# Kernel optimization log

Measured on AMD Instinct MI355X. Metric: run time of the kernel, lower is better.

Reference implementation:

```python
import jax, jax.numpy as jnp
import numpy as np
from jax import lax

B, H, W = 4096, 15, 15
P, V = 16, 32
D = P + V            # 48
PCODE = 2380
NEMB = 2 * (PCODE + 1)  # 4762


def _conv(x, w, b=None, groups=1, pad='SAME'):
    # x: [B,C,H,W], w: [O, I/groups, kh, kw] (torch OIHW layout)
    y = lax.conv_general_dilated(
        x, w, window_strides=(1, 1), padding=pad,
        dimension_numbers=('NCHW', 'OIHW', 'NCHW'),
        feature_group_count=groups)
    if b is not None:
        y = y + b[None, :, None, None]
    return y


def setup_inputs() -> dict:
    key = jax.random.key(0)
    ks = jax.random.split(key, 18)
    f = lambda k, shape: (jax.random.normal(k, shape, jnp.float32) * 0.05)
    inp = {
        'emb': f(ks[0], (NEMB, D)),
        'conv_w': f(ks[1], (D, 1, 3, 3)),      # depthwise, groups=D
        'conv_b': f(ks[2], (D,)),
        'ppw_w': f(ks[3], (P, P, 1, 1)),
        'ppw_b': f(ks[4], (P,)),
        'pdw_w': f(ks[5], (P, 1, 3, 3)),       # depthwise, groups=P
        'pdw_b': f(ks[6], (P,)),
        'pf_w': f(ks[7], (1, P, 1, 1)),        # final policy conv, no bias
        'vpw_w': f(ks[8], (V, V, 1, 1)),
        'vpw_b': f(ks[9], (V,)),
        'vl1_w': f(ks[10], (V, V)),
        'vl1_b': f(ks[11], (V,)),
        'vl2_w': f(ks[12], (V, V)),
        'vl2_b': f(ks[13], (V,)),
        'vf_w': f(ks[14], (3, V)),
        'vf_b': f(ks[15], (3,)),
        'sparse_feature_input': jax.random.randint(ks[16], (B, 12, H, W), 0, PCODE, jnp.int32),
        'board_input': jax.random.randint(ks[17], (B, 2, H, W), 0, 2, jnp.int32),
    }
    return inp


def reference(emb, conv_w, conv_b, ppw_w, ppw_b, pdw_w, pdw_b, pf_w,
              vpw_w, vpw_b, vl1_w, vl1_b, vl2_w, vl2_b, vf_w, vf_b,
              sparse_feature_input, board_input):
    relu = jax.nn.relu
    # --- PatternCodeEmbedding ---
    pcode = sparse_feature_input[:, 10:12]                     # [B,2,H,W]
    pcode = jnp.where(board_input > 0, PCODE, pcode)
    pcode = pcode + jnp.array([0, PCODE + 1], jnp.int32)[None, :, None, None]
    feat = emb[pcode].sum(axis=1)                              # [B,H,W,D]
    feat = jnp.transpose(feat, (0, 3, 1, 2))                   # [B,D,H,W]
    # --- trunk depthwise conv ---
    feat = relu(_conv(feat, conv_w, conv_b, groups=D))
    # --- policy head ---
    pol = feat[:, :P]
    pol = relu(_conv(pol, ppw_w, ppw_b))
    pol = relu(_conv(pol, pdw_w, pdw_b, groups=P))
    pol = _conv(pol, pf_w)                                     # [B,1,H,W]
    # --- value head ---
    val = feat[:, P:]
    val = relu(_conv(val, vpw_w, vpw_b))
    val = jnp.mean(val, axis=(2, 3))                           # [B,V]
    val = relu(val @ vl1_w.T + vl1_b)
    val = relu(val @ vl2_w.T + vl2_b)
    val = val @ vf_w.T + vf_b                                  # [B,3]
    return val, pol
```

## Files before the change

### kernel.cpp

```cpp
#include <hip/hip_runtime.h>
#include <hip/hip_fp16.h>

typedef _Float16 half8  __attribute__((ext_vector_type(8)));
typedef _Float16 half4_t __attribute__((ext_vector_type(4)));
typedef _Float16 half2_t __attribute__((ext_vector_type(2)));
typedef float f32x4 __attribute__((ext_vector_type(4)));

namespace {
constexpr int NT = 256;
constexpr int NPIX = 225;
constexpr int PCODE_C = 2380;

constexpr int AROW = 272;
constexpr int ACG  = 4080;

constexpr int OFF_A     = 0;
constexpr int OFF_POLA0 = 0;
constexpr int OFF_XLO   = 12240;
constexpr int OFF_SV    = 23040;
constexpr int OFF_H1    = 23168;
constexpr int OFF_H2    = 23296;
constexpr int OFF_XHI   = 24480;
constexpr int OFF_ZROW  = 35280;
constexpr int OFF_WS    = 35392;
constexpr int OFF_SLOTP = 36352;
constexpr int SMEM_BYTES = 36672;
}

__device__ __forceinline__ half2_t pkrtz(float a, float b) {
    return __builtin_bit_cast(half2_t, __builtin_amdgcn_cvt_pkrtz(a, b));
}
__device__ __forceinline__ void wave_fence() {
    asm volatile("s_waitcnt lgkmcnt(0)" ::: "memory");
}

__global__ __launch_bounds__(NT, 4) void patnet_kernel(
    const float* __restrict__ emb,
    const float* __restrict__ conv_w, const float* __restrict__ conv_b,
    const float* __restrict__ ppw_w,  const float* __restrict__ ppw_b,
    const float* __restrict__ pdw_w,  const float* __restrict__ pdw_b,
    const float* __restrict__ pf_w,
    const float* __restrict__ vpw_w,  const float* __restrict__ vpw_b,
    const float* __restrict__ vl1_w,  const float* __restrict__ vl1_b,
    const float* __restrict__ vl2_w,  const float* __restrict__ vl2_b,
    const float* __restrict__ vf_w,   const float* __restrict__ vf_b,
    const int* __restrict__ sparse,   const int* __restrict__ board,
    float* __restrict__ out, int batch)
{
    __shared__ __align__(16) unsigned char smem[SMEM_BYTES];
    const int tid  = threadIdx.x;
    const int b    = blockIdx.x;
    const int lane = tid & 63;
    const int wave = tid >> 6;

    int c0 = 0, c1 = 0;
    if (tid < NPIX) {
        int s10 = sparse[b * 2700 + 10 * NPIX + tid];
        int s11 = sparse[b * 2700 + 11 * NPIX + tid];
        int b0  = board[b * 450 + tid];
        int b1  = board[b * 450 + NPIX + tid];
        c0 = (b0 > 0) ? PCODE_C : s10;
        c1 = ((b1 > 0) ? PCODE_C : s11) + (PCODE_C + 1);
    }

    {
        _Float16* WS = (_Float16*)(smem + OFF_WS);
        for (int i = tid; i < 480; i += NT) {
            int cg = i / 80, r = i - cg * 80;
            _Float16 v;
            if (r < 72) { int t = r >> 3, j = r & 7; v = (_Float16)conv_w[(cg * 8 + j) * 9 + t]; }
            else        { v = (_Float16)conv_b[cg * 8 + (r - 72)]; }
            WS[i] = v;
        }
        _Float16* WP = (_Float16*)(smem + OFF_SLOTP);
        if (tid < 160) {
            int cg = tid / 80, r = tid - cg * 80;
            _Float16 v;
            if (r < 72) { int t = r >> 3, j = r & 7; v = (_Float16)pdw_w[(cg * 8 + j) * 9 + t]; }
            else        { v = (_Float16)pdw_b[cg * 8 + (r - 72)]; }
            WP[tid] = v;
        }
        if (tid < 187) {
            unsigned char* dst;
            if (tid < 180) {
                int cg = tid / 30, r = tid - cg * 30;
                int row = r >> 1, colB = (r & 1) * 256;
                dst = smem + OFF_A + cg * ACG + row * AROW + colB;
            } else {
                dst = smem + OFF_ZROW + (tid - 180) * 16;
            }
            *(half8*)dst = (half8)(_Float16)0.f;
        }
    }

    if (tid < NPIX) {
        const float* e0 = emb + c0 * 48;
        const float* e1 = emb + c1 * 48;
        int y = tid / 15, x = tid - y * 15;
        unsigned char* abase = smem + OFF_A + y * AROW + (x + 1) * 16;
        #pragma unroll
        for (int g = 0; g < 6; g++) {
            f32x4 x0 = *(const f32x4*)(e0 + g * 8);
            f32x4 x1 = *(const f32x4*)(e0 + g * 8 + 4);
            f32x4 y0 = *(const f32x4*)(e1 + g * 8);
            f32x4 y1 = *(const f32x4*)(e1 + g * 8 + 4);
            f32x4 s0 = x0 + y0, s1 = x1 + y1;
            half2_t q0 = pkrtz(s0.x, s0.y), q1 = pkrtz(s0.z, s0.w);
            half2_t q2 = pkrtz(s1.x, s1.y), q3 = pkrtz(s1.z, s1.w);
            half8 hv = {q0[0], q0[1], q1[0], q1[1], q2[0], q2[1], q3[0], q3[1]};
            *(half8*)(abase + g * ACG) = hv;
        }
    }
    __syncthreads();

    auto do_strip = [&](int t, int cgbase, int xBase) {
        int cgl = t / 75, rem = t - cgl * 75;
        int y = rem / 5, s = rem - y * 5;
        int cg = cgbase + cgl;
        const unsigned char* wb = smem + OFF_WS + cg * 160;
        half8 wv[9];
        #pragma unroll
        for (int i = 0; i < 9; i++) wv[i] = *(const half8*)(wb + i * 16);
        half8 bias = *(const half8*)(wb + 144);
        const unsigned char* abase = smem + OFF_A + cg * ACG;
        int xo = s * 48;
        const unsigned char* r0 = (y >= 1)  ? abase + (y - 1) * AROW + xo : smem + OFF_ZROW;
        const unsigned char* r1 = abase + y * AROW + xo;
        const unsigned char* r2 = (y <= 13) ? abase + (y + 1) * AROW + xo : smem + OFF_ZROW;
        half8 acc[3] = {bias, bias, bias};
        #pragma unroll
        for (int c = 0; c < 5; c++) {
            half8 v0 = *(const half8*)(r0 + c * 16);
            half8 v1 = *(const half8*)(r1 + c * 16);
            half8 v2 = *(const half8*)(r2 + c * 16);
            #pragma unroll
            for (int o = 0; o < 3; o++) {
                int kx = c - o;
                if (kx >= 0 && kx <= 2) {
                    acc[o] = __builtin_elementwise_fma(v0, wv[kx],     acc[o]);
                    acc[o] = __builtin_elementwise_fma(v1, wv[3 + kx], acc[o]);
                    acc[o] = __builtin_elementwise_fma(v2, wv[6 + kx], acc[o]);
                }
            }
        }
        unsigned char* xw = smem + xBase + (y * 15 + s * 3) * 48 + cgl * 16;
        #pragma unroll
        for (int o = 0; o < 3; o++)
            *(half8*)(xw + o * 48) = __builtin_elementwise_max(acc[o], (half8)(_Float16)0.f);
    };

    if (tid < 225) do_strip(tid, 3, OFF_XHI);
    __syncthreads();
    if (tid < 225) do_strip(tid, 0, OFF_XLO);

    const int n = lane & 15, q = lane >> 4;
    const int cgp = lane & 1;
    half8 af_p;
    {
        const float* wp = ppw_w + n * 16 + (q & 1) * 8;
        f32x4 w0 = *(const f32x4*)wp, w1 = *(const f32x4*)(wp + 4);
        half8 t = {(_Float16)w0.x, (_Float16)w0.y, (_Float16)w0.z, (_Float16)w0.w,
                   (_Float16)w1.x, (_Float16)w1.y, (_Float16)w1.z, (_Float16)w1.w};
        af_p = (q < 2) ? t : (half8)(_Float16)0.f;
    }
    f32x4 pb = *(const f32x4*)(ppw_b + q * 4);
    half2_t pf0 = pkrtz(pf_w[cgp * 8 + 0], pf_w[cgp * 8 + 1]);
    half2_t pf1 = pkrtz(pf_w[cgp * 8 + 2], pf_w[cgp * 8 + 3]);
    half2_t pf2 = pkrtz(pf_w[cgp * 8 + 4], pf_w[cgp * 8 + 5]);
    half2_t pf3 = pkrtz(pf_w[cgp * 8 + 6], pf_w[cgp * 8 + 7]);
    half8 af0, af1;
    {
        const float* wp = vpw_w + n * 32 + q * 8;
        f32x4 w0 = *(const f32x4*)wp, w1 = *(const f32x4*)(wp + 4);
        af0 = half8{(_Float16)w0.x, (_Float16)w0.y, (_Float16)w0.z, (_Float16)w0.w,
                    (_Float16)w1.x, (_Float16)w1.y, (_Float16)w1.z, (_Float16)w1.w};
        const float* wp2 = vpw_w + (16 + n) * 32 + q * 8;
        f32x4 v0 = *(const f32x4*)wp2, v1 = *(const f32x4*)(wp2 + 4);
        af1 = half8{(_Float16)v0.x, (_Float16)v0.y, (_Float16)v0.z, (_Float16)v0.w,
                    (_Float16)v1.x, (_Float16)v1.y, (_Float16)v1.z, (_Float16)v1.w};
    }
    f32x4 vb0 = *(const f32x4*)(vpw_b + q * 4);
    f32x4 vb1 = *(const f32x4*)(vpw_b + 16 + q * 4);
    __syncthreads();

    if (wave < 3) {
        if (lane < 60) {
            int cg = lane / 30, r = lane - cg * 30;
            int row = r >> 1, colB = (r & 1) * 256;
            *(half8*)(smem + OFF_POLA0 + cg * ACG + row * AROW + colB) = (half8)(_Float16)0.f;
        }
        half8 wvp[9];
        #pragma unroll
        for (int t = 0; t < 9; t++) wvp[t] = *(const half8*)(smem + OFF_SLOTP + cgp * 160 + t * 16);
        half8 biasp = *(const half8*)(smem + OFF_SLOTP + cgp * 160 + 144);

        const int tlo = (wave == 0) ? 0 : ((wave == 1) ? 3 : 8);
        const int thi = (wave == 0) ? 6 : ((wave == 1) ? 11 : 15);
        const int cg3 = q >> 1;
        const int xoff = (q & 1) * 16;
        for (int t = tlo; t < thi; t++) {
            int p = t * 16 + n;
            int pc = (p > 224) ? 224 : p;
            half8 bf = *(const half8*)(smem + OFF_XLO + pc * 48 + xoff);
            f32x4 d = __builtin_amdgcn_mfma_f32_16x16x32_f16(af_p, bf, (f32x4)(0.f), 0, 0, 0);
            if (p < NPIX) {
                int y = p / 15, x = p - y * 15;
                half2_t lo = pkrtz(fmaxf(d.x + pb.x, 0.f), fmaxf(d.y + pb.y, 0.f));
                half2_t hi = pkrtz(fmaxf(d.z + pb.z, 0.f), fmaxf(d.w + pb.w, 0.f));
                half4_t hv = {lo[0], lo[1], hi[0], hi[1]};
                *(half4_t*)(smem + OFF_POLA0 + cg3 * ACG + y * AROW + (x + 1) * 16 + (q & 1) * 8) = hv;
            }
        }
        wave_fence();

        const int px0 = wave * 75;
        for (int i = 0; i < 3; i++) {
            int idx = i * 64 + lane;
            if (idx < 150) {
                int px = px0 + (idx >> 1);
                int y = px / 15, x = px - y * 15;
                const unsigned char* base = smem + OFF_POLA0 + cgp * ACG;
                int xo = x * 16;
                const unsigned char* pm = (y > 0)  ? base + (y - 1) * AROW + xo : smem + OFF_ZROW;
                const unsigned char* pz = base + y * AROW + xo;
                const unsigned char* pp = (y < 14) ? base + (y + 1) * AROW + xo : smem + OFF_ZROW;
                half8 acc = biasp;
                acc = __builtin_elementwise_fma(*(const half8*)(pm),      wvp[0], acc);
                acc = __builtin_elementwise_fma(*(const half8*)(pm + 16), wvp[1], acc);
                acc = __builtin_elementwise_fma(*(const half8*)(pm + 32), wvp[2], acc);
                acc = __builtin_elementwise_fma(*(const half8*)(pz),      wvp[3], acc);
                acc = __builtin_elementwise_fma(*(const half8*)(pz + 16), wvp[4], acc);
                acc = __builtin_elementwise_fma(*(const half8*)(pz + 32), wvp[5], acc);
                acc = __builtin_elementwise_fma(*(const half8*)(pp),      wvp[6], acc);
                acc = __builtin_elementwise_fma(*(const half8*)(pp + 16), wvp[7], acc);
                acc = __builtin_elementwise_fma(*(const half8*)(pp + 32), wvp[8], acc);
                acc = __builtin_elementwise_max(acc, (half8)(_Float16)0.f);
                float part = 0.f;
                part = __builtin_amdgcn_fdot2(half2_t{acc[0], acc[1]}, pf0, part, false);
                part = __builtin_amdgcn_fdot2(half2_t{acc[2], acc[3]}, pf1, part, false);
                part = __builtin_amdgcn_fdot2(half2_t{acc[4], acc[5]}, pf2, part, false);
                part = __builtin_amdgcn_fdot2(half2_t{acc[6], acc[7]}, pf3, part, false);
                float tot = part + __shfl_xor(part, 1, 64);
                if (cgp == 0) out[3 * batch + b * NPIX + px] = tot;
            }
        }
    } else {
        const int xb = (q == 0) ? (OFF_XLO + 32) : (OFF_XHI + (q - 1) * 16);
        f32x4 a0 = {0.f, 0.f, 0.f, 0.f}, a1 = {0.f, 0.f, 0.f, 0.f};
        for (int t = 0; t < 15; t++) {
            int p = t * 16 + n;
            int pc = (p > 224) ? 224 : p;
            half8 bf = *(const half8*)(smem + xb + pc * 48);
            f32x4 d0 = __builtin_amdgcn_mfma_f32_16x16x32_f16(af0, bf, (f32x4)(0.f), 0, 0, 0);
            f32x4 d1 = __builtin_amdgcn_mfma_f32_16x16x32_f16(af1, bf, (f32x4)(0.f), 0, 0, 0);
            if (p < NPIX) {
                #pragma unroll
                for (int r = 0; r < 4; r++) {
                    a0[r] += fmaxf(d0[r] + vb0[r], 0.f);
                    a1[r] += fmaxf(d1[r] + vb1[r], 0.f);
                }
            }
        }
        #pragma unroll
        for (int s = 1; s < 16; s <<= 1) {
            #pragma unroll
            for (int r = 0; r < 4; r++) {
                a0[r] += __shfl_xor(a0[r], s, 64);
                a1[r] += __shfl_xor(a1[r], s, 64);
            }
        }
        if (n == 0) {
            *(f32x4*)(smem + OFF_SV + q * 16)      = a0 * (1.f / 225.f);
            *(f32x4*)(smem + OFF_SV + 64 + q * 16) = a1 * (1.f / 225.f);
        }
        const int o = lane & 31;
        f32x4 wA[8];
        float b1v = vl1_b[o], b2v = vl2_b[o], b3v = 0.f;
        #pragma unroll
        for (int g = 0; g < 8; g++) wA[g] = *(const f32x4*)(vl1_w + o * 32 + g * 4);
        wave_fence();

        f32x4 wB[8];
        #pragma unroll
        for (int g = 0; g < 8; g++) wB[g] = *(const f32x4*)(vl2_w + o * 32 + g * 4);
        float acc1 = b1v;
        #pragma unroll
        for (int g = 0; g < 8; g++) {
            f32x4 sv = *(const f32x4*)(smem + OFF_SV + g * 16);
            acc1 += sv.x * wA[g].x + sv.y * wA[g].y + sv.z * wA[g].z + sv.w * wA[g].w;
        }
        acc1 = fmaxf(acc1, 0.f);
        if (lane < 32) *(float*)(smem + OFF_H1 + o * 4) = acc1;
        wave_fence();

        f32x4 wC[8];
        if (lane < 3) {
            b3v = vf_b[lane];
            #pragma unroll
            for (int g = 0; g < 8; g++) wC[g] = *(const f32x4*)(vf_w + lane * 32 + g * 4);
        }
        float acc2 = b2v;
        #pragma unroll
        for (int g = 0; g < 8; g++) {
            f32x4 hv = *(const f32x4*)(smem + OFF_H1 + g * 16);
            acc2 += hv.x * wB[g].x + hv.y * wB[g].y + hv.z * wB[g].z + hv.w * wB[g].w;
        }
        acc2 = fmaxf(acc2, 0.f);
        if (lane < 32) *(float*)(smem + OFF_H2 + o * 4) = acc2;
        wave_fence();

        if (lane < 3) {
            float acc3 = b3v;
            #pragma unroll
            for (int g = 0; g < 8; g++) {
                f32x4 hv = *(const f32x4*)(smem + OFF_H2 + g * 16);
                acc3 += hv.x * wC[g].x + hv.y * wC[g].y + hv.z * wC[g].z + hv.w * wC[g].w;
            }
            out[b * 3 + lane] = acc3;
        }
    }
}

extern "C" void kernel_launch(void* const* d_in, const int* in_sizes, int n_in,
                              void* d_out, int out_size, void* d_ws, size_t ws_size,
                              hipStream_t stream) {
    const float* emb    = (const float*)d_in[0];
    const float* conv_w = (const float*)d_in[1];
    const float* conv_b = (const float*)d_in[2];
    const float* ppw_w  = (const float*)d_in[3];
    const float* ppw_b  = (const float*)d_in[4];
    const float* pdw_w  = (const float*)d_in[5];
    const float* pdw_b  = (const float*)d_in[6];
    const float* pf_w   = (const float*)d_in[7];
    const float* vpw_w  = (const float*)d_in[8];
    const float* vpw_b  = (const float*)d_in[9];
    const float* vl1_w  = (const float*)d_in[10];
    const float* vl1_b  = (const float*)d_in[11];
    const float* vl2_w  = (const float*)d_in[12];
    const float* vl2_b  = (const float*)d_in[13];
    const float* vf_w   = (const float*)d_in[14];
    const float* vf_b   = (const float*)d_in[15];
    const int* sparse   = (const int*)d_in[16];
    const int* board    = (const int*)d_in[17];
    float* out = (float*)d_out;

    int batch = in_sizes[16] / 2700;
    patnet_kernel<<<batch, NT, 0, stream>>>(
        emb, conv_w, conv_b, ppw_w, ppw_b, pdw_w, pdw_b, pf_w,
        vpw_w, vpw_b, vl1_w, vl1_b, vl2_w, vl2_b, vf_w, vf_b,
        sparse, board, out, batch);
}
```

Baseline: 165.5 us.

## Split depthwise trunk conv between policy and value waves, widen strips to 5 pixels

The trunk depthwise conv is restructured. Value-channel groups are computed by 180 threads before the barrier. Each policy wave computes the policy-channel strips for its own rows after the barrier, so one __syncthreads is removed and the policy conv runs alongside the value head. Strips now produce 5 outputs per thread instead of 3, which reuses more loaded input. The output uses a per-channel-group planar layout, which adds LDS. A risk is that policy waves may read rows that neighbouring waves compute, since only a wave-local fence is used.

```diff
diff --git a/kernel.cpp b/kernel.cpp
--- a/kernel.cpp
+++ b/kernel.cpp
@@ -15,16 +15,16 @@
 constexpr int ACG  = 4080;
 
 constexpr int OFF_A     = 0;
-constexpr int OFF_POLA0 = 0;
-constexpr int OFF_XLO   = 12240;
-constexpr int OFF_SV    = 23040;
-constexpr int OFF_H1    = 23168;
-constexpr int OFF_H2    = 23296;
+constexpr int OFF_XLO   = 8160;
+constexpr int OFF_SV    = 15360;
+constexpr int OFF_H1    = 15488;
+constexpr int OFF_H2    = 15616;
+constexpr int OFF_POLA  = 16320;
 constexpr int OFF_XHI   = 24480;
-constexpr int OFF_ZROW  = 35280;
-constexpr int OFF_WS    = 35392;
-constexpr int OFF_SLOTP = 36352;
-constexpr int SMEM_BYTES = 36672;
+constexpr int OFF_ZROW  = 38880;
+constexpr int OFF_WS    = 38992;
+constexpr int OFF_SLOTP = 39952;
+constexpr int SMEM_BYTES = 40272;
 }
 
 __device__ __forceinline__ half2_t pkrtz(float a, float b) {
@@ -113,28 +113,25 @@
     }
     __syncthreads();
 
-    auto do_strip = [&](int t, int cgbase, int xBase) {
-        int cgl = t / 75, rem = t - cgl * 75;
-        int y = rem / 5, s = rem - y * 5;
-        int cg = cgbase + cgl;
+    auto strip5 = [&](int cg, int y, int s, unsigned char* plane) {
         const unsigned char* wb = smem + OFF_WS + cg * 160;
         half8 wv[9];
         #pragma unroll
         for (int i = 0; i < 9; i++) wv[i] = *(const half8*)(wb + i * 16);
         half8 bias = *(const half8*)(wb + 144);
         const unsigned char* abase = smem + OFF_A + cg * ACG;
-        int xo = s * 48;
+        int xo = s * 80;
         const unsigned char* r0 = (y >= 1)  ? abase + (y - 1) * AROW + xo : smem + OFF_ZROW;
         const unsigned char* r1 = abase + y * AROW + xo;
         const unsigned char* r2 = (y <= 13) ? abase + (y + 1) * AROW + xo : smem + OFF_ZROW;
-        half8 acc[3] = {bias, bias, bias};
-        #pragma unroll
-        for (int c = 0; c < 5; c++) {
+        half8 acc[5] = {bias, bias, bias, bias, bias};
+        #pragma unroll
+        for (int c = 0; c < 7; c++) {
             half8 v0 = *(const half8*)(r0 + c * 16);
             half8 v1 = *(const half8*)(r1 + c * 16);
             half8 v2 = *(const half8*)(r2 + c * 16);
             #pragma unroll
-            for (int o = 0; o < 3; o++) {
+            for (int o = 0; o < 5; o++) {
                 int kx = c - o;
                 if (kx >= 0 && kx <= 2) {
                     acc[o] = __builtin_elementwise_fma(v0, wv[kx],     acc[o]);
@@ -143,15 +140,17 @@
                 }
             }
         }
-        unsigned char* xw = smem + xBase + (y * 15 + s * 3) * 48 + cgl * 16;
-        #pragma unroll
-        for (int o = 0; o < 3; o++)
-            *(half8*)(xw + o * 48) = __builtin_elementwise_max(acc[o], (half8)(_Float16)0.f);
+        unsigned char* xw = plane + (y * 15 + s * 5) * 16;
+        #pragma unroll
+        for (int o = 0; o < 5; o++)
+            *(half8*)(xw + o * 16) = __builtin_elementwise_max(acc[o], (half8)(_Float16)0.f);
     };
 
-    if (tid < 225) do_strip(tid, 3, OFF_XHI);
-    __syncthreads();
-    if (tid < 225) do_strip(tid, 0, OFF_XLO);
+    if (tid < 180) {
+        int cgl = tid / 45, rem = tid - cgl * 45;
+        int y = rem / 3, s = rem - y * 3;
+        strip5(2 + cgl, y, s, smem + OFF_XHI + cgl * 3600);
+    }
 
     const int n = lane & 15, q = lane >> 4;
     const int cgp = lane & 1;
@@ -184,31 +183,39 @@
     __syncthreads();
 
     if (wave < 3) {
+        const int r0w = (wave == 0) ? 0 : ((wave == 1) ? 3 : 8);
+        const int nr  = (wave == 1) ? 9 : 7;
+        if (lane < 2 * nr * 3) {
+            int cgl = lane / (nr * 3), rem = lane - cgl * (nr * 3);
+            int yy = r0w + rem / 3, ss = rem - (rem / 3) * 3;
+            strip5(cgl, yy, ss, smem + OFF_XLO + cgl * 3600);
+        }
         if (lane < 60) {
             int cg = lane / 30, r = lane - cg * 30;
             int row = r >> 1, colB = (r & 1) * 256;
-            *(half8*)(smem + OFF_POLA0 + cg * ACG + row * AROW + colB) = (half8)(_Float16)0.f;
+            *(half8*)(smem + OFF_POLA + cg * ACG + row * AROW + colB) = (half8)(_Float16)0.f;
         }
         half8 wvp[9];
         #pragma unroll
         for (int t = 0; t < 9; t++) wvp[t] = *(const half8*)(smem + OFF_SLOTP + cgp * 160 + t * 16);
         half8 biasp = *(const half8*)(smem + OFF_SLOTP + cgp * 160 + 144);
+        wave_fence();
 
         const int tlo = (wave == 0) ? 0 : ((wave == 1) ? 3 : 8);
         const int thi = (wave == 0) ? 6 : ((wave == 1) ? 11 : 15);
         const int cg3 = q >> 1;
-        const int xoff = (q & 1) * 16;
+        const unsigned char* xlp = smem + OFF_XLO + (q & 1) * 3600;
         for (int t = tlo; t < thi; t++) {
             int p = t * 16 + n;
             int pc = (p > 224) ? 224 : p;
-            half8 bf = *(const half8*)(smem + OFF_XLO + pc * 48 + xoff);
+            half8 bf = *(const half8*)(xlp + pc * 16);
             f32x4 d = __builtin_amdgcn_mfma_f32_16x16x32_f16(af_p, bf, (f32x4)(0.f), 0, 0, 0);
             if (p < NPIX) {
                 int y = p / 15, x = p - y * 15;
                 half2_t lo = pkrtz(fmaxf(d.x + pb.x, 0.f), fmaxf(d.y + pb.y, 0.f));
                 half2_t hi = pkrtz(fmaxf(d.z + pb.z, 0.f), fmaxf(d.w + pb.w, 0.f));
                 half4_t hv = {lo[0], lo[1], hi[0], hi[1]};
-                *(half4_t*)(smem + OFF_POLA0 + cg3 * ACG + y * AROW + (x + 1) * 16 + (q & 1) * 8) = hv;
+                *(half4_t*)(smem + OFF_POLA + cg3 * ACG + y * AROW + (x + 1) * 16 + (q & 1) * 8) = hv;
             }
         }
         wave_fence();
@@ -219,7 +226,7 @@
             if (idx < 150) {
                 int px = px0 + (idx >> 1);
                 int y = px / 15, x = px - y * 15;
-                const unsigned char* base = smem + OFF_POLA0 + cgp * ACG;
+                const unsigned char* base = smem + OFF_POLA + cgp * ACG;
                 int xo = x * 16;
                 const unsigned char* pm = (y > 0)  ? base + (y - 1) * AROW + xo : smem + OFF_ZROW;
                 const unsigned char* pz = base + y * AROW + xo;
@@ -245,12 +252,12 @@
             }
         }
     } else {
-        const int xb = (q == 0) ? (OFF_XLO + 32) : (OFF_XHI + (q - 1) * 16);
+        const unsigned char* xb = smem + OFF_XHI + q * 3600;
         f32x4 a0 = {0.f, 0.f, 0.f, 0.f}, a1 = {0.f, 0.f, 0.f, 0.f};
         for (int t = 0; t < 15; t++) {
             int p = t * 16 + n;
             int pc = (p > 224) ? 224 : p;
-            half8 bf = *(const half8*)(smem + xb + pc * 48);
+            half8 bf = *(const half8*)(xb + pc * 16);
             f32x4 d0 = __builtin_amdgcn_mfma_f32_16x16x32_f16(af0, bf, (f32x4)(0.f), 0, 0, 0);
             f32x4 d1 = __builtin_amdgcn_mfma_f32_16x16x32_f16(af1, bf, (f32x4)(0.f), 0, 0, 0);
             if (p < NPIX) {
```

Result: no change. 168.3 us (+1.7%).

## Process two batch samples per 512-thread block with split shared memory

Applied to the files above, without the earlier changes.

Each block now handles two batch elements, with 8 waves split into two halves that each run the original 4-wave pipeline on their own shared-memory region. Conv and pointwise weights and the zero row are staged once per block and shared by both halves, which halves the per-sample weight staging and the block launch count. In exchange, shared memory per block roughly doubles, launch bounds drop to 2 blocks per CU, and every __syncthreads now has to wait for both samples, so the two halves run in lockstep.

```diff
diff --git a/kernel.cpp b/kernel.cpp
--- a/kernel.cpp
+++ b/kernel.cpp
@@ -7,24 +7,26 @@
 typedef float f32x4 __attribute__((ext_vector_type(4)));
 
 namespace {
-constexpr int NT = 256;
+constexpr int NT = 512;
 constexpr int NPIX = 225;
 constexpr int PCODE_C = 2380;
 
 constexpr int AROW = 272;
 constexpr int ACG  = 4080;
+constexpr int BRD  = 35280;
 
 constexpr int OFF_A     = 0;
-constexpr int OFF_POLA0 = 0;
+constexpr int OFF_POLA  = 0;
 constexpr int OFF_XLO   = 12240;
 constexpr int OFF_SV    = 23040;
 constexpr int OFF_H1    = 23168;
 constexpr int OFF_H2    = 23296;
 constexpr int OFF_XHI   = 24480;
-constexpr int OFF_ZROW  = 35280;
-constexpr int OFF_WS    = 35392;
-constexpr int OFF_SLOTP = 36352;
-constexpr int SMEM_BYTES = 36672;
+
+constexpr int OFF_ZROW  = 70560;
+constexpr int OFF_WS    = 70672;
+constexpr int OFF_SLOTP = 71632;
+constexpr int SMEM_BYTES = 71952;
 }
 
 __device__ __forceinline__ half2_t pkrtz(float a, float b) {
@@ -34,7 +36,7 @@
     asm volatile("s_waitcnt lgkmcnt(0)" ::: "memory");
 }
 
-__global__ __launch_bounds__(NT, 4) void patnet_kernel(
+__global__ __launch_bounds__(NT, 2) void patnet_kernel(
     const float* __restrict__ emb,
     const float* __restrict__ conv_w, const float* __restrict__ conv_b,
     const float* __restrict__ ppw_w,  const float* __restrict__ ppw_b,
@@ -49,28 +51,33 @@
 {
     __shared__ __align__(16) unsigned char smem[SMEM_BYTES];
     const int tid  = threadIdx.x;
-    const int b    = blockIdx.x;
     const int lane = tid & 63;
     const int wave = tid >> 6;
+    const int role = wave & 3;
+    const int half = wave >> 2;
+    const int t8   = tid & 255;
+    const int b    = blockIdx.x * 2 + half;
+    const bool bok = (b < batch);
+    unsigned char* const bs = smem + half * BRD;
 
     int c0 = 0, c1 = 0;
-    if (tid < NPIX) {
-        int s10 = sparse[b * 2700 + 10 * NPIX + tid];
-        int s11 = sparse[b * 2700 + 11 * NPIX + tid];
-        int b0  = board[b * 450 + tid];
-        int b1  = board[b * 450 + NPIX + tid];
+    if (t8 < NPIX && bok) {
+        int s10 = sparse[b * 2700 + 10 * NPIX + t8];
+        int s11 = sparse[b * 2700 + 11 * NPIX + t8];
+        int b0  = board[b * 450 + t8];
+        int b1  = board[b * 450 + NPIX + t8];
         c0 = (b0 > 0) ? PCODE_C : s10;
         c1 = ((b1 > 0) ? PCODE_C : s11) + (PCODE_C + 1);
     }
 
     {
         _Float16* WS = (_Float16*)(smem + OFF_WS);
-        for (int i = tid; i < 480; i += NT) {
-            int cg = i / 80, r = i - cg * 80;
+        if (tid < 480) {
+            int cg = tid / 80, r = tid - cg * 80;
             _Float16 v;
             if (r < 72) { int t = r >> 3, j = r & 7; v = (_Float16)conv_w[(cg * 8 + j) * 9 + t]; }
             else        { v = (_Float16)conv_b[cg * 8 + (r - 72)]; }
-            WS[i] = v;
+            WS[tid] = v;
         }
         _Float16* WP = (_Float16*)(smem + OFF_SLOTP);
         if (tid < 160) {
@@ -80,24 +87,25 @@
             else        { v = (_Float16)pdw_b[cg * 8 + (r - 72)]; }
             WP[tid] = v;
         }
-        if (tid < 187) {
+        if (tid < 367) {
             unsigned char* dst;
-            if (tid < 180) {
-                int cg = tid / 30, r = tid - cg * 30;
+            if (tid < 360) {
+                int hb = tid / 180, i = tid - hb * 180;
+                int cg = i / 30, r = i - cg * 30;
                 int row = r >> 1, colB = (r & 1) * 256;
-                dst = smem + OFF_A + cg * ACG + row * AROW + colB;
+                dst = smem + hb * BRD + OFF_A + cg * ACG + row * AROW + colB;
             } else {
-                dst = smem + OFF_ZROW + (tid - 180) * 16;
+                dst = smem + OFF_ZROW + (tid - 360) * 16;
             }
             *(half8*)dst = (half8)(_Float16)0.f;
         }
     }
 
-    if (tid < NPIX) {
+    if (t8 < NPIX) {
         const float* e0 = emb + c0 * 48;
         const float* e1 = emb + c1 * 48;
-        int y = tid / 15, x = tid - y * 15;
-        unsigned char* abase = smem + OFF_A + y * AROW + (x + 1) * 16;
+        int y = t8 / 15, x = t8 - y * 15;
+        unsigned char* abase = bs + OFF_A + y * AROW + (x + 1) * 16;
         #pragma unroll
         for (int g = 0; g < 6; g++) {
             f32x4 x0 = *(const f32x4*)(e0 + g * 8);
@@ -122,7 +130,7 @@
         #pragma unroll
         for (int i = 0; i < 9; i++) wv[i] = *(const half8*)(wb + i * 16);
         half8 bias = *(const half8*)(wb + 144);
-        const unsigned char* abase = smem + OFF_A + cg * ACG;
+        const unsigned char* abase = bs + OFF_A + cg * ACG;
         int xo = s * 48;
         const unsigned char* r0 = (y >= 1)  ? abase + (y - 1) * AROW + xo : smem + OFF_ZROW;
         const unsigned char* r1 = abase + y * AROW + xo;
@@ -143,15 +151,15 @@
                 }
             }
         }
-        unsigned char* xw = smem + xBase + (y * 15 + s * 3) * 48 + cgl * 16;
+        unsigned char* xw = bs + xBase + (y * 15 + s * 3) * 48 + cgl * 16;
         #pragma unroll
         for (int o = 0; o < 3; o++)
             *(half8*)(xw + o * 48) = __builtin_elementwise_max(acc[o], (half8)(_Float16)0.f);
     };
 
-    if (tid < 225) do_strip(tid, 3, OFF_XHI);
+    if (t8 < 225) do_strip(t8, 3, OFF_XHI);
     __syncthreads();
-    if (tid < 225) do_strip(tid, 0, OFF_XLO);
+    if (t8 < 225) do_strip(t8, 0, OFF_XLO);
 
     const int n = lane & 15, q = lane >> 4;
     const int cgp = lane & 1;
@@ -183,43 +191,43 @@
     f32x4 vb1 = *(const f32x4*)(vpw_b + 16 + q * 4);
     __syncthreads();
 
-    if (wave < 3) {
+    if (role < 3) {
         if (lane < 60) {
             int cg = lane / 30, r = lane - cg * 30;
             int row = r >> 1, colB = (r & 1) * 256;
-            *(half8*)(smem + OFF_POLA0 + cg * ACG + row * AROW + colB) = (half8)(_Float16)0.f;
+            *(half8*)(bs + OFF_POLA + cg * ACG + row * AROW + colB) = (half8)(_Float16)0.f;
         }
         half8 wvp[9];
         #pragma unroll
         for (int t = 0; t < 9; t++) wvp[t] = *(const half8*)(smem + OFF_SLOTP + cgp * 160 + t * 16);
         half8 biasp = *(const half8*)(smem + OFF_SLOTP + cgp * 160 + 144);
 
-        const int tlo = (wave == 0) ? 0 : ((wave == 1) ? 3 : 8);
-        const int thi = (wave == 0) ? 6 : ((wave == 1) ? 11 : 15);
+        const int tlo = (role == 0) ? 0 : ((role == 1) ? 3 : 8);
+        const int thi = (role == 0) ? 6 : ((role == 1) ? 11 : 15);
         const int cg3 = q >> 1;
         const int xoff = (q & 1) * 16;
         for (int t = tlo; t < thi; t++) {
             int p = t * 16 + n;
             int pc = (p > 224) ? 224 : p;
-            half8 bf = *(const half8*)(smem + OFF_XLO + pc * 48 + xoff);
+            half8 bf = *(const half8*)(bs + OFF_XLO + pc * 48 + xoff);
             f32x4 d = __builtin_amdgcn_mfma_f32_16x16x32_f16(af_p, bf, (f32x4)(0.f), 0, 0, 0);
             if (p < NPIX) {
                 int y = p / 15, x = p - y * 15;
                 half2_t lo = pkrtz(fmaxf(d.x + pb.x, 0.f), fmaxf(d.y + pb.y, 0.f));
                 half2_t hi = pkrtz(fmaxf(d.z + pb.z, 0.f), fmaxf(d.w + pb.w, 0.f));
                 half4_t hv = {lo[0], lo[1], hi[0], hi[1]};
-                *(half4_t*)(smem + OFF_POLA0 + cg3 * ACG + y * AROW + (x + 1) * 16 + (q & 1) * 8) = hv;
+                *(half4_t*)(bs + OFF_POLA + cg3 * ACG + y * AROW + (x + 1) * 16 + (q & 1) * 8) = hv;
             }
         }
         wave_fence();
 
-        const int px0 = wave * 75;
+        const int px0 = role * 75;
         for (int i = 0; i < 3; i++) {
             int idx = i * 64 + lane;
             if (idx < 150) {
                 int px = px0 + (idx >> 1);
                 int y = px / 15, x = px - y * 15;
-                const unsigned char* base = smem + OFF_POLA0 + cgp * ACG;
+                const unsigned char* base = bs + OFF_POLA + cgp * ACG;
                 int xo = x * 16;
                 const unsigned char* pm = (y > 0)  ? base + (y - 1) * AROW + xo : smem + OFF_ZROW;
                 const unsigned char* pz = base + y * AROW + xo;
@@ -241,16 +249,16 @@
                 part = __builtin_amdgcn_fdot2(half2_t{acc[4], acc[5]}, pf2, part, false);
                 part = __builtin_amdgcn_fdot2(half2_t{acc[6], acc[7]}, pf3, part, false);
                 float tot = part + __shfl_xor(part, 1, 64);
-                if (cgp == 0) out[3 * batch + b * NPIX + px] = tot;
+                if (cgp == 0 && bok) out[3 * batch + b * NPIX + px] = tot;
             }
         }
     } else {
-        const int xb = (q == 0) ? (OFF_XLO + 32) : (OFF_XHI + (q - 1) * 16);
+        const unsigned char* xb = bs + ((q == 0) ? (OFF_XLO + 32) : (OFF_XHI + (q - 1) * 16));
         f32x4 a0 = {0.f, 0.f, 0.f, 0.f}, a1 = {0.f, 0.f, 0.f, 0.f};
         for (int t = 0; t < 15; t++) {
             int p = t * 16 + n;
             int pc = (p > 224) ? 224 : p;
-            half8 bf = *(const half8*)(smem + xb + pc * 48);
+            half8 bf = *(const half8*)(xb + pc * 48);
             f32x4 d0 = __builtin_amdgcn_mfma_f32_16x16x32_f16(af0, bf, (f32x4)(0.f), 0, 0, 0);
             f32x4 d1 = __builtin_amdgcn_mfma_f32_16x16x32_f16(af1, bf, (f32x4)(0.f), 0, 0, 0);
             if (p < NPIX) {
@@ -270,8 +278,8 @@
             }
         }
         if (n == 0) {
-            *(f32x4*)(smem + OFF_SV + q * 16)      = a0 * (1.f / 225.f);
-            *(f32x4*)(smem + OFF_SV + 64 + q * 16) = a1 * (1.f / 225.f);
+            *(f32x4*)(bs + OFF_SV + q * 16)      = a0 * (1.f / 225.f);
+            *(f32x4*)(bs + OFF_SV + 64 + q * 16) = a1 * (1.f / 225.f);
         }
         const int o = lane & 31;
         f32x4 wA[8];
@@ -286,11 +294,11 @@
         float acc1 = b1v;
         #pragma unroll
         for (int g = 0; g < 8; g++) {
-            f32x4 sv = *(const f32x4*)(smem + OFF_SV + g * 16);
+            f32x4 sv = *(const f32x4*)(bs + OFF_SV + g * 16);
             acc1 += sv.x * wA[g].x + sv.y * wA[g].y + sv.z * wA[g].z + sv.w * wA[g].w;
         }
         acc1 = fmaxf(acc1, 0.f);
-        if (lane < 32) *(float*)(smem + OFF_H1 + o * 4) = acc1;
+        if (lane < 32) *(float*)(bs + OFF_H1 + o * 4) = acc1;
         wave_fence();
 
         f32x4 wC[8];
@@ -302,18 +310,18 @@
         float acc2 = b2v;
         #pragma unroll
         for (int g = 0; g < 8; g++) {
-            f32x4 hv = *(const f32x4*)(smem + OFF_H1 + g * 16);
+            f32x4 hv = *(const f32x4*)(bs + OFF_H1 + g * 16);
             acc2 += hv.x * wB[g].x + hv.y * wB[g].y + hv.z * wB[g].z + hv.w * wB[g].w;
         }
         acc2 = fmaxf(acc2, 0.f);
-        if (lane < 32) *(float*)(smem + OFF_H2 + o * 4) = acc2;
+        if (lane < 32) *(float*)(bs + OFF_H2 + o * 4) = acc2;
         wave_fence();
 
-        if (lane < 3) {
+        if (lane < 3 && bok) {
             float acc3 = b3v;
             #pragma unroll
             for (int g = 0; g < 8; g++) {
-                f32x4 hv = *(const f32x4*)(smem + OFF_H2 + g * 16);
+                f32x4 hv = *(const f32x4*)(bs + OFF_H2 + g * 16);
                 acc3 += hv.x * wC[g].x + hv.y * wC[g].y + hv.z * wC[g].z + hv.w * wC[g].w;
             }
             out[b * 3 + lane] = acc3;
@@ -345,7 +353,8 @@
     float* out = (float*)d_out;
 
     int batch = in_sizes[16] / 2700;
-    patnet_kernel<<<batch, NT, 0, stream>>>(
+    int grid = (batch + 1) / 2;
+    patnet_kernel<<<grid, NT, 0, stream>>>(
         emb, conv_w, conv_b, ppw_w, ppw_b, pdw_w, pdw_b, pf_w,
         vpw_w, vpw_b, vl1_w, vl1_b, vl2_w, vl2_b, vf_w, vf_b,
         sparse, board, out, batch);
```

New measurement: 169.6 us. 1.02x slower.
